# Performance work log

Hardware: AMD Instinct MI355X
Metric: run time of the kernel (lower is better)

## Reference

```python
import jax, jax.numpy as jnp
import numpy as np

N = 50000          # points
K = 16             # neighbors per query (n_max)
M = N * K          # ragged pair count
DIM = 96
HEADS = 6
HEAD_DIM = DIM // HEADS
WINDOW = 4.0
QUANT = 0.25
QGL = int(WINDOW / QUANT)   # quant_grid_length = 16
SCALE = HEAD_DIM ** -0.5


def setup_inputs() -> dict:
    key = jax.random.key(0)
    ks = jax.random.split(key, 10)
    feats = jax.random.normal(ks[0], (N, DIM), dtype=jnp.float32)
    xyz = jax.random.uniform(ks[1], (N, 3), dtype=jnp.float32) * 8.0
    index_0 = jnp.repeat(jnp.arange(N, dtype=jnp.int32), K)            # sorted query ids
    index_1 = jax.random.randint(ks[2], (M,), 0, N, dtype=jnp.int32)   # neighbor ids
    index_0_offsets = jnp.arange(N + 1, dtype=jnp.int32) * K
    W_qkv = jax.random.normal(ks[3], (DIM, 3 * DIM), dtype=jnp.float32) * 0.02
    b_qkv = jnp.zeros((3 * DIM,), dtype=jnp.float32)
    table_q = jax.random.normal(ks[4], (4 * QGL, HEADS, HEAD_DIM, 3), dtype=jnp.float32) * 0.02
    table_k = jax.random.normal(ks[5], (4 * QGL, HEADS, HEAD_DIM, 3), dtype=jnp.float32) * 0.02
    table_v = jax.random.normal(ks[6], (4 * QGL, HEADS, HEAD_DIM, 3), dtype=jnp.float32) * 0.02
    W_proj = jax.random.normal(ks[7], (DIM, DIM), dtype=jnp.float32) * 0.02
    b_proj = jnp.zeros((DIM,), dtype=jnp.float32)
    return {
        "feats": feats, "xyz": xyz,
        "index_0": index_0, "index_0_offsets": index_0_offsets, "n_max": K,
        "index_1": index_1, "shift_size": jnp.float32(0.0),
        "W_qkv": W_qkv, "b_qkv": b_qkv,
        "table_q": table_q, "table_k": table_k, "table_v": table_v,
        "W_proj": W_proj, "b_proj": b_proj,
    }


def reference(feats, xyz, index_0, index_0_offsets, n_max, index_1, shift_size,
              W_qkv, b_qkv, table_q, table_k, table_v, W_proj, b_proj):
    n = feats.shape[0]
    # qkv projection -> (N, 3, H, HD)
    qkv = (feats @ W_qkv + b_qkv).reshape(n, 3, HEADS, HEAD_DIM)
    q = qkv[:, 0] * SCALE
    k = qkv[:, 1]
    v = qkv[:, 2]

    # step1: per-pair QK dot product (pointops.attention_step1_v2)
    qg = q[index_0]                      # (M, H, HD) gathered by query id
    kg = k[index_1]                      # (M, H, HD) gathered by neighbor id
    attn = jnp.einsum('mhd,mhd->mh', qg, kg)   # (M, H)

    # quantized relative positions
    xyz_quant = jnp.floor(((xyz - xyz.min(axis=0) + shift_size) % WINDOW) / QUANT)
    rel = xyz_quant[index_0] - xyz_quant[index_1]       # (M, 3)
    rel_idx = (rel + (QGL - 1)).astype(jnp.int32)       # map_func, in [0, 2*QGL-2]

    # relative position bias (pointops.dot_prod_with_idx_v3: query + key tables)
    bias = jnp.zeros_like(attn)
    for c in range(3):   # fixed 3 coordinate axes
        tq = table_q[rel_idx[:, c], :, :, c]            # (M, H, HD)
        tk = table_k[rel_idx[:, c], :, :, c]
        bias = bias + jnp.einsum('mhd,mhd->mh', qg, tq) + jnp.einsum('mhd,mhd->mh', kg, tk)
    attn = attn + bias

    # scatter softmax over index_0 segments
    seg_max = jax.ops.segment_max(attn, index_0, num_segments=n)
    e = jnp.exp(attn - seg_max[index_0])
    denom = jax.ops.segment_sum(e, index_0, num_segments=n)
    sm = e / denom[index_0]                              # (M, H)

    # step2 with relative position value (pointops.attention_step2_with_rel_pos_value_v2)
    vg = v[index_1]                                      # (M, H, HD)
    for c in range(3):
        vg = vg + table_v[rel_idx[:, c], :, :, c]
    x = jax.ops.segment_sum(sm[:, :, None] * vg, index_0, num_segments=n)  # (N, H, HD)
    x = x.reshape(n, DIM)
    return x @ W_proj + b_proj
```

## Files before the change

kernel.cpp:

```cpp
#include <hip/hip_runtime.h>
#include <hip/hip_fp16.h>
#include <math.h>

#define FLT_BIG 3.402823466e38f
typedef unsigned int uint;
typedef unsigned short ushort;
typedef __attribute__((ext_vector_type(8))) _Float16 half8;
typedef __attribute__((ext_vector_type(4))) float floatx4;

__device__ inline ushort f2h(float f) {
    return __half_as_ushort(__float2half(f));
}
__device__ inline float dot2(uint a, uint b, float c) {
    float d;
    asm("v_dot2_f32_f16 %0, %1, %2, %3" : "=v"(d) : "v"(a), "v"(b), "v"(c));
    return d;
}
template <int CTRL>
__device__ inline float dppf(float x) {
    return __int_as_float(__builtin_amdgcn_update_dpp(
        __float_as_int(x), __float_as_int(x), CTRL, 0xF, 0xF, true));
}

__global__ void min_reduce_kernel(const float* __restrict__ xyz, int n, float* mn) {
    float m0 = FLT_BIG, m1 = FLT_BIG, m2 = FLT_BIG;
    for (int i = blockIdx.x * blockDim.x + threadIdx.x; i < n; i += gridDim.x * blockDim.x) {
        m0 = fminf(m0, xyz[3 * i + 0]);
        m1 = fminf(m1, xyz[3 * i + 1]);
        m2 = fminf(m2, xyz[3 * i + 2]);
    }
#pragma unroll
    for (int off = 32; off > 0; off >>= 1) {
        m0 = fminf(m0, __shfl_down(m0, off));
        m1 = fminf(m1, __shfl_down(m1, off));
        m2 = fminf(m2, __shfl_down(m2, off));
    }
    if ((threadIdx.x & 63) == 0) {
        atomicMin((int*)&mn[0], __float_as_int(m0));
        atomicMin((int*)&mn[1], __float_as_int(m1));
        atomicMin((int*)&mn[2], __float_as_int(m2));
    }
}

__global__ void prep_kernel(const float* __restrict__ W_qkv,
                            const float* __restrict__ W_proj,
                            const float* __restrict__ tq, const float* __restrict__ tk,
                            const float* __restrict__ tv,
                            ushort* __restrict__ wtqkv, ushort* __restrict__ wtproj,
                            ushort* __restrict__ rq, ushort* __restrict__ rk,
                            ushort* __restrict__ rv, float* mn) {
    int tid = blockIdx.x * 256 + threadIdx.x;
    if (tid < 3) mn[tid] = FLT_BIG;
    if (tid < 18432) {
        int c = tid / 6144, rem = tid - c * 6144;
        int idx = rem / 96, hd = rem - idx * 96;
        int src = (idx * 96 + hd) * 3 + c;
        rq[tid] = f2h(tq[src]);
        rk[tid] = f2h(tk[src]);
        rv[tid] = f2h(tv[src]);
    }
    if (tid < 27648) {
        int j = tid / 96, d = tid - j * 96;
        wtqkv[tid] = f2h(W_qkv[d * 288 + j]);
    }
    if (tid < 9216) {
        int j = tid / 96, d = tid - j * 96;
        wtproj[tid] = f2h(W_proj[d * 96 + j]);
    }
}

__global__ __launch_bounds__(256) void qkv_mfma_kernel(
    const float* __restrict__ A, const ushort* __restrict__ WT,
    const float* __restrict__ bias, uint4* __restrict__ qout4,
    uint4* __restrict__ kvout4, const float* __restrict__ xyz,
    const float* __restrict__ mn, const float* __restrict__ shiftp,
    uint* __restrict__ xq, int n) {
    __shared__ ushort lds[4][32 * 112];
    const int wave = threadIdx.x >> 6, lane = threadIdx.x & 63;
    const int ch = blockIdx.y;
    const int m = lane & 15, q = lane >> 4;
    const int row0 = blockIdx.x * 128 + wave * 32;
    if (row0 >= n) return;

    if (ch == 0 && threadIdx.x < 128) {
        int rp = blockIdx.x * 128 + threadIdx.x;
        if (rp < n) {
            float shift = shiftp[0];
            float q0 = floorf(fmodf(xyz[3 * rp + 0] - mn[0] + shift, 4.0f) * 4.0f);
            float q1 = floorf(fmodf(xyz[3 * rp + 1] - mn[1] + shift, 4.0f) * 4.0f);
            float q2 = floorf(fmodf(xyz[3 * rp + 2] - mn[2] + shift, 4.0f) * 4.0f);
            xq[rp] = (uint)(int)q0 | ((uint)(int)q1 << 8) | ((uint)(int)q2 << 16);
        }
    }

    const ushort* wbase = WT + ((size_t)ch * 96 + m) * 96 + q * 8;
    int r0 = row0 + m;      if (r0 > n - 1) r0 = n - 1;
    int r1 = row0 + 16 + m; if (r1 > n - 1) r1 = n - 1;
    const float4* A4 = (const float4*)A;

    floatx4 acc[2][6];
#pragma unroll
    for (int g = 0; g < 2; g++)
#pragma unroll
        for (int ct = 0; ct < 6; ct++) acc[g][ct] = (floatx4){0.f, 0.f, 0.f, 0.f};

#pragma unroll
    for (int kk4 = 0; kk4 < 24; kk4 += 8) {
        float4 fa = A4[(size_t)r0 * 24 + kk4 + q * 2];
        float4 fb = A4[(size_t)r0 * 24 + kk4 + q * 2 + 1];
        float4 ga = A4[(size_t)r1 * 24 + kk4 + q * 2];
        float4 gb = A4[(size_t)r1 * 24 + kk4 + q * 2 + 1];
        half8 a0, a1;
        a0[0] = (_Float16)fa.x; a0[1] = (_Float16)fa.y; a0[2] = (_Float16)fa.z; a0[3] = (_Float16)fa.w;
        a0[4] = (_Float16)fb.x; a0[5] = (_Float16)fb.y; a0[6] = (_Float16)fb.z; a0[7] = (_Float16)fb.w;
        a1[0] = (_Float16)ga.x; a1[1] = (_Float16)ga.y; a1[2] = (_Float16)ga.z; a1[3] = (_Float16)ga.w;
        a1[4] = (_Float16)gb.x; a1[5] = (_Float16)gb.y; a1[6] = (_Float16)gb.z; a1[7] = (_Float16)gb.w;
#pragma unroll
        for (int ct = 0; ct < 6; ct++) {
            half8 b = *(const half8*)(wbase + ct * 16 * 96 + kk4 * 4);
            acc[0][ct] = __builtin_amdgcn_mfma_f32_16x16x32_f16(a0, b, acc[0][ct], 0, 0, 0);
            acc[1][ct] = __builtin_amdgcn_mfma_f32_16x16x32_f16(a1, b, acc[1][ct], 0, 0, 0);
        }
    }

    ushort* L = lds[wave];
    const float sc = (ch == 0) ? 0.25f : 1.0f;
#pragma unroll
    for (int g = 0; g < 2; g++)
#pragma unroll
        for (int ct = 0; ct < 6; ct++) {
            float bv = bias[ch * 96 + ct * 16 + m];
#pragma unroll
            for (int r = 0; r < 4; r++) {
                int rowl = g * 16 + q * 4 + r;
                L[rowl * 112 + ct * 16 + m] = f2h((acc[g][ct][r] + bv) * sc);
            }
        }
    const int strideU4 = (ch == 0) ? 12 : 24;
    const int offU4 = (ch == 2) ? 12 : 0;
    uint4* dst = (ch == 0) ? qout4 : kvout4;
#pragma unroll
    for (int i = 0; i < 6; i++) {
        int idx = i * 64 + lane;
        int rowl = idx / 12, u4 = idx - rowl * 12;
        int grow = row0 + rowl;
        if (grow < n) {
            uint4 val = *(const uint4*)(L + rowl * 112 + u4 * 8);
            dst[(size_t)grow * strideU4 + offU4 + u4] = val;
        }
    }
}

__global__ __launch_bounds__(256) void proj_mfma_kernel(
    const ushort* __restrict__ A, const ushort* __restrict__ WT,
    const float* __restrict__ bias, float* __restrict__ out, int n) {
    const int wave = threadIdx.x >> 6, lane = threadIdx.x & 63;
    const int m = lane & 15, q = lane >> 4;
    const int row0 = blockIdx.x * 128 + wave * 32;
    if (row0 >= n) return;

    const ushort* wbase = WT + (size_t)m * 96 + q * 8;
    int r0 = row0 + m;      if (r0 > n - 1) r0 = n - 1;
    int r1 = row0 + 16 + m; if (r1 > n - 1) r1 = n - 1;

    floatx4 acc[2][6];
#pragma unroll
    for (int g = 0; g < 2; g++)
#pragma unroll
        for (int ct = 0; ct < 6; ct++) acc[g][ct] = (floatx4){0.f, 0.f, 0.f, 0.f};

#pragma unroll
    for (int kk = 0; kk < 96; kk += 32) {
        half8 a0 = *(const half8*)(A + (size_t)r0 * 96 + q * 8 + kk);
        half8 a1 = *(const half8*)(A + (size_t)r1 * 96 + q * 8 + kk);
#pragma unroll
        for (int ct = 0; ct < 6; ct++) {
            half8 b = *(const half8*)(wbase + ct * 16 * 96 + kk);
            acc[0][ct] = __builtin_amdgcn_mfma_f32_16x16x32_f16(a0, b, acc[0][ct], 0, 0, 0);
            acc[1][ct] = __builtin_amdgcn_mfma_f32_16x16x32_f16(a1, b, acc[1][ct], 0, 0, 0);
        }
    }

#pragma unroll
    for (int g = 0; g < 2; g++)
#pragma unroll
        for (int ct = 0; ct < 6; ct++) {
            int col = ct * 16 + m;
            float bv = bias[col];
#pragma unroll
            for (int r = 0; r < 4; r++) {
                int row = row0 + g * 16 + q * 4 + r;
                if (row < n) out[(size_t)row * 96 + col] = acc[g][ct][r] + bv;
            }
        }
}

#define ATTN_NB 256
#define ATTN_B 8
__global__ __launch_bounds__(768) void attn_kernel(
    const ushort* __restrict__ qh, const ushort* __restrict__ kv,
    const uint* __restrict__ xq, const int* __restrict__ index_1,
    const ushort* __restrict__ rq, const ushort* __restrict__ rk,
    const ushort* __restrict__ rv, ushort* __restrict__ xout, int n) {
    __shared__ uint4 ldsraw[6912];
    char* Lb = (char*)ldsraw;

    const int t = threadIdx.x;
    const int pt = t / 96, tp = t - pt * 96;
    const int h = tp >> 4, e = tp & 15;

    const int stride = gridDim.x * ATTN_B;
    const int iters = (n + stride - 1) / stride;

    int pA, jdA; uint xqpA;
    auto PREF_A = [&](int it) {
        pA = (it * gridDim.x + blockIdx.x) * ATTN_B + pt;
        int pc = pA < n ? pA : n - 1;
        jdA = index_1[(size_t)pc * 16 + e];
        xqpA = xq[pc];
    };
    int p, jd; uint xqp, xqj;
    uint4 ka, kb, va, vb, qa, qb;
    auto PREF_B = [&]() {
        p = pA; jd = jdA; xqp = xqpA;
        int pc = p < n ? p : n - 1;
        const ushort* row = kv + (size_t)jd * 192;
        ka = *(const uint4*)(row + h * 16);
        kb = *(const uint4*)(row + h * 16 + 8);
        va = *(const uint4*)(row + 96 + h * 16);
        vb = *(const uint4*)(row + 96 + h * 16 + 8);
        const ushort* qrow = qh + (size_t)pc * 96 + h * 16;
        qa = *(const uint4*)qrow;
        qb = *(const uint4*)(qrow + 8);
        xqj = xq[jd];
    };
    PREF_A(0); PREF_B(); PREF_A(1);

#pragma unroll
    for (int j = 0; j < 9; j++) {
        const uint4* src = (j < 3) ? (const uint4*)rq
                         : (j < 6) ? (const uint4*)rk : (const uint4*)rv;
        int rem = t + (j % 3) * 768;
        int ROW = rem / 12, slot = rem - ROW * 12;
        uint4 val = src[rem];
        *(uint4*)(Lb + (j / 3) * 36864 + ROW * 192 +
                  ((slot << 4) ^ (((ROW >> 1) & 3) << 4))) = val;
    }
    __syncthreads();

    auto LD2 = [&](const char* base, int R, uint4& A, uint4& B) {
        int x = ((R >> 1) & 3) << 4;
        const char* rb = base + R * 192;
        A = *(const uint4*)(rb + ((h * 32) ^ x));
        B = *(const uint4*)(rb + ((h * 32 + 16) ^ x));
    };
    auto F2 = [](const uint4& u, int i) -> float2 {
        return __half22float2(((const __half2*)&u)[i]);
    };

    const bool b3 = (e & 8) != 0, b2 = (e & 4) != 0;
    const bool b1 = (e & 2) != 0, b0 = (e & 1) != 0;

    for (int it = 0; it < iters; it++) {
        const int i0 = (int)(xqp & 255u) - (int)(xqj & 255u) + 15;
        const int i1 = (int)((xqp >> 8) & 255u) - (int)((xqj >> 8) & 255u) + 15;
        const int i2 = (int)((xqp >> 16) & 255u) - (int)((xqj >> 16) & 255u) + 15;

        float f[16];
#pragma unroll
        for (int i = 0; i < 4; i++) {
            float2 lo = F2(va, i), hi = F2(vb, i);
            f[2 * i] = lo.x; f[2 * i + 1] = lo.y;
            f[8 + 2 * i] = hi.x; f[8 + 2 * i + 1] = hi.y;
        }

        float a;
        {
            float x0 = dot2(qa.x, ka.x, 0.f), x1 = dot2(qa.y, ka.y, 0.f);
            x0 = dot2(qa.z, ka.z, x0); x1 = dot2(qa.w, ka.w, x1);
            x0 = dot2(qb.x, kb.x, x0); x1 = dot2(qb.y, kb.y, x1);
            x0 = dot2(qb.z, kb.z, x0); x1 = dot2(qb.w, kb.w, x1);
            float bias = 0.f;
#define BIAS_C(ROW)                                                            \
            {                                                                  \
                uint4 ta, tb, ua, ub;                                          \
                LD2(Lb, (ROW), ta, tb);                                        \
                LD2(Lb + 36864, (ROW), ua, ub);                                \
                float u = dot2(qa.x, ta.x, 0.f), w = dot2(ka.x, ua.x, 0.f);    \
                u = dot2(qa.y, ta.y, u); w = dot2(ka.y, ua.y, w);              \
                u = dot2(qa.z, ta.z, u); w = dot2(ka.z, ua.z, w);              \
                u = dot2(qa.w, ta.w, u); w = dot2(ka.w, ua.w, w);              \
                u = dot2(qb.x, tb.x, u); w = dot2(kb.x, ub.x, w);              \
                u = dot2(qb.y, tb.y, u); w = dot2(kb.y, ub.y, w);              \
                u = dot2(qb.z, tb.z, u); w = dot2(kb.z, ub.z, w);              \
                u = dot2(qb.w, tb.w, u); w = dot2(kb.w, ub.w, w);              \
                bias += u + w;                                                 \
            }
            BIAS_C(i0)
            BIAS_C(64 + i1)
            BIAS_C(128 + i2)
#undef BIAS_C
            a = x0 + x1 + bias;
        }

        const int op = p;
        if (it + 1 < iters) { PREF_B(); PREF_A(it + 2); }

        {
            uint4 t0a, t0b, t1a, t1b, t2a, t2b;
            LD2(Lb + 73728, i0, t0a, t0b);
            LD2(Lb + 73728, 64 + i1, t1a, t1b);
            LD2(Lb + 73728, 128 + i2, t2a, t2b);
#pragma unroll
            for (int i = 0; i < 4; i++) {
                float2 a0 = F2(t0a, i), a1 = F2(t1a, i), a2 = F2(t2a, i);
                f[2 * i]     += a0.x + a1.x + a2.x;
                f[2 * i + 1] += a0.y + a1.y + a2.y;
                float2 c0 = F2(t0b, i), c1 = F2(t1b, i), c2 = F2(t2b, i);
                f[8 + 2 * i]     += c0.x + c1.x + c2.x;
                f[8 + 2 * i + 1] += c0.y + c1.y + c2.y;
            }
        }

        float wgt;
        {
            float mx = a;
            mx = fmaxf(mx, dppf<0x128>(mx));
            mx = fmaxf(mx, dppf<0x124>(mx));
            mx = fmaxf(mx, dppf<0x122>(mx));
            mx = fmaxf(mx, dppf<0x121>(mx));
            float ex = __expf(a - mx);
            float sum = ex;
            sum += dppf<0x128>(sum);
            sum += dppf<0x124>(sum);
            sum += dppf<0x122>(sum);
            sum += dppf<0x121>(sum);
            wgt = ex * __builtin_amdgcn_rcpf(sum);
        }

        float P[16];
#pragma unroll
        for (int c = 0; c < 16; c++) P[c] = wgt * f[c];
        float A8[8];
#pragma unroll
        for (int j = 0; j < 8; j++) {
            float kp = b3 ? P[j + 8] : P[j];
            float sd = b3 ? P[j] : P[j + 8];
            A8[j] = kp + dppf<0x140>(sd);
        }
        float B4[4];
#pragma unroll
        for (int j = 0; j < 4; j++) {
            float kp = b2 ? A8[j + 4] : A8[j];
            float sd = b2 ? A8[j] : A8[j + 4];
            B4[j] = kp + dppf<0x141>(sd);
        }
        float C2[2];
#pragma unroll
        for (int j = 0; j < 2; j++) {
            float kp = b1 ? B4[j + 2] : B4[j];
            float sd = b1 ? B4[j] : B4[j + 2];
            C2[j] = kp + dppf<0x4E>(sd);
        }
        {
            float kp = b0 ? C2[1] : C2[0];
            float sd = b0 ? C2[0] : C2[1];
            float xres = kp + dppf<0xB1>(sd);
            if (op < n) xout[(size_t)op * 96 + tp] = f2h(xres);
        }
    }
}

extern "C" void kernel_launch(void* const* d_in, const int* in_sizes, int n_in,
                              void* d_out, int out_size, void* d_ws, size_t ws_size,
                              hipStream_t stream) {
    const float* feats   = (const float*)d_in[0];
    const float* xyz     = (const float*)d_in[1];
    const int*   index_1 = (const int*)d_in[5];
    const float* shiftp  = (const float*)d_in[6];
    const float* W_qkv   = (const float*)d_in[7];
    const float* b_qkv   = (const float*)d_in[8];
    const float* table_q = (const float*)d_in[9];
    const float* table_k = (const float*)d_in[10];
    const float* table_v = (const float*)d_in[11];
    const float* W_proj  = (const float*)d_in[12];
    const float* b_proj  = (const float*)d_in[13];
    float* out = (float*)d_out;

    const int n = in_sizes[0] / 96;

    float* w = (float*)d_ws;
    float*  mn     = w;
    ushort* qbf    = (ushort*)(w + 16);
    ushort* kvbuf  = qbf + (size_t)n * 96;
    ushort* xbuf   = kvbuf + (size_t)n * 192;
    ushort* wtqkv  = xbuf + (size_t)n * 96;
    ushort* wtproj = wtqkv + 27648;
    ushort* rq     = wtproj + 9216;
    ushort* rk     = rq + 18432;
    ushort* rv     = rk + 18432;
    uint*   xqv    = (uint*)(rv + 18432);

    const int GB = (n + 127) / 128;

    prep_kernel<<<108, 256, 0, stream>>>(W_qkv, W_proj, table_q, table_k, table_v,
                                         wtqkv, wtproj, rq, rk, rv, mn);
    min_reduce_kernel<<<256, 256, 0, stream>>>(xyz, n, mn);
    qkv_mfma_kernel<<<dim3(GB, 3), 256, 0, stream>>>(feats, wtqkv, b_qkv,
                                                     (uint4*)qbf, (uint4*)kvbuf,
                                                     xyz, mn, shiftp, xqv, n);
    attn_kernel<<<ATTN_NB, 768, 0, stream>>>(qbf, kvbuf, xqv, index_1, rq, rk,
                                             rv, xbuf, n);
    proj_mfma_kernel<<<GB, 256, 0, stream>>>(xbuf, wtproj, b_proj, out, n);
}
```

Measured before the change: 225.0 us.

## Stage fp16 feature tile in LDS shared by q/k/v waves; pad attention table rows

Result: no change. 225.6 us (+0.3%).

```diff
diff --git a/kernel.cpp b/kernel.cpp
--- a/kernel.cpp
+++ b/kernel.cpp
@@ -69,21 +69,19 @@
     }
 }
 
-__global__ __launch_bounds__(256) void qkv_mfma_kernel(
+__global__ __launch_bounds__(384) void qkv_mfma_kernel(
     const float* __restrict__ A, const ushort* __restrict__ WT,
     const float* __restrict__ bias, uint4* __restrict__ qout4,
     uint4* __restrict__ kvout4, const float* __restrict__ xyz,
     const float* __restrict__ mn, const float* __restrict__ shiftp,
     uint* __restrict__ xq, int n) {
-    __shared__ ushort lds[4][32 * 112];
-    const int wave = threadIdx.x >> 6, lane = threadIdx.x & 63;
-    const int ch = blockIdx.y;
-    const int m = lane & 15, q = lane >> 4;
-    const int row0 = blockIdx.x * 128 + wave * 32;
-    if (row0 >= n) return;
-
-    if (ch == 0 && threadIdx.x < 128) {
-        int rp = blockIdx.x * 128 + threadIdx.x;
+    __shared__ ushort Ash[64 * 104];
+    __shared__ ushort lds[6][32 * 112];
+    const int t = threadIdx.x;
+    const int row0 = blockIdx.x * 64;
+
+    if (t < 64) {
+        int rp = row0 + t;
         if (rp < n) {
             float shift = shiftp[0];
             float q0 = floorf(fmodf(xyz[3 * rp + 0] - mn[0] + shift, 4.0f) * 4.0f);
@@ -93,10 +91,26 @@
         }
     }
 
+    const float4* A4 = (const float4*)A;
+#pragma unroll
+    for (int j = 0; j < 4; j++) {
+        int idx = t + j * 384;
+        int row = idx / 24, c4 = idx - row * 24;
+        int gr = row0 + row; if (gr > n - 1) gr = n - 1;
+        float4 v = A4[(size_t)gr * 24 + c4];
+        uint2 pk;
+        pk.x = (uint)f2h(v.x) | ((uint)f2h(v.y) << 16);
+        pk.y = (uint)f2h(v.z) | ((uint)f2h(v.w) << 16);
+        *(uint2*)&Ash[row * 104 + c4 * 4] = pk;
+    }
+    __syncthreads();
+
+    const int wave = t >> 6, lane = t & 63;
+    const int ch = wave >> 1, rg = wave & 1;
+    const int m = lane & 15, q = lane >> 4;
+    const int wrow0 = row0 + rg * 32;
+
     const ushort* wbase = WT + ((size_t)ch * 96 + m) * 96 + q * 8;
-    int r0 = row0 + m;      if (r0 > n - 1) r0 = n - 1;
-    int r1 = row0 + 16 + m; if (r1 > n - 1) r1 = n - 1;
-    const float4* A4 = (const float4*)A;
 
     floatx4 acc[2][6];
 #pragma unroll
@@ -106,15 +120,8 @@
 
 #pragma unroll
     for (int kk4 = 0; kk4 < 24; kk4 += 8) {
-        float4 fa = A4[(size_t)r0 * 24 + kk4 + q * 2];
-        float4 fb = A4[(size_t)r0 * 24 + kk4 + q * 2 + 1];
-        float4 ga = A4[(size_t)r1 * 24 + kk4 + q * 2];
-        float4 gb = A4[(size_t)r1 * 24 + kk4 + q * 2 + 1];
-        half8 a0, a1;
-        a0[0] = (_Float16)fa.x; a0[1] = (_Float16)fa.y; a0[2] = (_Float16)fa.z; a0[3] = (_Float16)fa.w;
-        a0[4] = (_Float16)fb.x; a0[5] = (_Float16)fb.y; a0[6] = (_Float16)fb.z; a0[7] = (_Float16)fb.w;
-        a1[0] = (_Float16)ga.x; a1[1] = (_Float16)ga.y; a1[2] = (_Float16)ga.z; a1[3] = (_Float16)ga.w;
-        a1[4] = (_Float16)gb.x; a1[5] = (_Float16)gb.y; a1[6] = (_Float16)gb.z; a1[7] = (_Float16)gb.w;
+        half8 a0 = *(const half8*)&Ash[(rg * 32 + m) * 104 + (kk4 + q * 2) * 4];
+        half8 a1 = *(const half8*)&Ash[(rg * 32 + 16 + m) * 104 + (kk4 + q * 2) * 4];
 #pragma unroll
         for (int ct = 0; ct < 6; ct++) {
             half8 b = *(const half8*)(wbase + ct * 16 * 96 + kk4 * 4);
@@ -143,7 +150,7 @@
     for (int i = 0; i < 6; i++) {
         int idx = i * 64 + lane;
         int rowl = idx / 12, u4 = idx - rowl * 12;
-        int grow = row0 + rowl;
+        int grow = wrow0 + rowl;
         if (grow < n) {
             uint4 val = *(const uint4*)(L + rowl * 112 + u4 * 8);
             dst[(size_t)grow * strideU4 + offU4 + u4] = val;
@@ -197,12 +204,14 @@
 
 #define ATTN_NB 256
 #define ATTN_B 8
+#define TPITCH 208
+#define TSIZE  39936
 __global__ __launch_bounds__(768) void attn_kernel(
     const ushort* __restrict__ qh, const ushort* __restrict__ kv,
     const uint* __restrict__ xq, const int* __restrict__ index_1,
     const ushort* __restrict__ rq, const ushort* __restrict__ rk,
     const ushort* __restrict__ rv, ushort* __restrict__ xout, int n) {
-    __shared__ uint4 ldsraw[6912];
+    __shared__ uint4 ldsraw[7488];
     char* Lb = (char*)ldsraw;
 
     const int t = threadIdx.x;
@@ -243,16 +252,14 @@
         int rem = t + (j % 3) * 768;
         int ROW = rem / 12, slot = rem - ROW * 12;
         uint4 val = src[rem];
-        *(uint4*)(Lb + (j / 3) * 36864 + ROW * 192 +
-                  ((slot << 4) ^ (((ROW >> 1) & 3) << 4))) = val;
+        *(uint4*)(Lb + (j / 3) * TSIZE + ROW * TPITCH + slot * 16) = val;
     }
     __syncthreads();
 
     auto LD2 = [&](const char* base, int R, uint4& A, uint4& B) {
-        int x = ((R >> 1) & 3) << 4;
-        const char* rb = base + R * 192;
-        A = *(const uint4*)(rb + ((h * 32) ^ x));
-        B = *(const uint4*)(rb + ((h * 32 + 16) ^ x));
+        const char* rb = base + R * TPITCH + h * 32;
+        A = *(const uint4*)rb;
+        B = *(const uint4*)(rb + 16);
     };
     auto F2 = [](const uint4& u, int i) -> float2 {
         return __half22float2(((const __half2*)&u)[i]);
@@ -285,7 +292,7 @@
             {                                                                  \
                 uint4 ta, tb, ua, ub;                                          \
                 LD2(Lb, (ROW), ta, tb);                                        \
-                LD2(Lb + 36864, (ROW), ua, ub);                                \
+                LD2(Lb + TSIZE, (ROW), ua, ub);                                \
                 float u = dot2(qa.x, ta.x, 0.f), w = dot2(ka.x, ua.x, 0.f);    \
                 u = dot2(qa.y, ta.y, u); w = dot2(ka.y, ua.y, w);              \
                 u = dot2(qa.z, ta.z, u); w = dot2(ka.z, ua.z, w);              \
@@ -308,9 +315,9 @@
 
         {
             uint4 t0a, t0b, t1a, t1b, t2a, t2b;
-            LD2(Lb + 73728, i0, t0a, t0b);
-            LD2(Lb + 73728, 64 + i1, t1a, t1b);
-            LD2(Lb + 73728, 128 + i2, t2a, t2b);
+            LD2(Lb + 2 * TSIZE, i0, t0a, t0b);
+            LD2(Lb + 2 * TSIZE, 64 + i1, t1a, t1b);
+            LD2(Lb + 2 * TSIZE, 128 + i2, t2a, t2b);
 #pragma unroll
             for (int i = 0; i < 4; i++) {
                 float2 a0 = F2(t0a, i), a1 = F2(t1a, i), a2 = F2(t2a, i);
@@ -401,15 +408,14 @@
     ushort* rv     = rk + 18432;
     uint*   xqv    = (uint*)(rv + 18432);
 
-    const int GB = (n + 127) / 128;
-
     prep_kernel<<<108, 256, 0, stream>>>(W_qkv, W_proj, table_q, table_k, table_v,
                                          wtqkv, wtproj, rq, rk, rv, mn);
     min_reduce_kernel<<<256, 256, 0, stream>>>(xyz, n, mn);
-    qkv_mfma_kernel<<<dim3(GB, 3), 256, 0, stream>>>(feats, wtqkv, b_qkv,
-                                                     (uint4*)qbf, (uint4*)kvbuf,
-                                                     xyz, mn, shiftp, xqv, n);
+    qkv_mfma_kernel<<<(n + 63) / 64, 384, 0, stream>>>(feats, wtqkv, b_qkv,
+                                                       (uint4*)qbf, (uint4*)kvbuf,
+                                                       xyz, mn, shiftp, xqv, n);
     attn_kernel<<<ATTN_NB, 768, 0, stream>>>(qbf, kvbuf, xqv, index_1, rq, rk,
                                              rv, xbuf, n);
-    proj_mfma_kernel<<<GB, 256, 0, stream>>>(xbuf, wtproj, b_proj, out, n);
-}
+    proj_mfma_kernel<<<(n + 127) / 128, 256, 0, stream>>>(xbuf, wtproj, b_proj,
+                                                          out, n);
+}
```
